# Kernel tuning notes

Measured on AMD Instinct MI355X. Metric: run time of the kernel, lower is better.

Reference implementation:

```python
import jax, jax.numpy as jnp
import numpy as np

NEG_SLOPE = 0.2
EPS = 1e-16


def _gat_conv(x, src, dst, edge_attr, W, We, att_src, att_dst, att_edge, bias):
    """PyG GATConv, heads=H, concat=False, edge_dim given. x:[N,F_in]."""
    N = x.shape[0]
    H, C = att_src.shape
    xs = (x @ W.T).reshape(N, H, C)                      # [N,H,C]
    a_src = jnp.einsum('nhc,hc->nh', xs, att_src)        # [N,H]
    a_dst = jnp.einsum('nhc,hc->nh', xs, att_dst)        # [N,H]
    e = (edge_attr @ We.T).reshape(-1, H, C)             # [E,H,C]
    a_edge = jnp.einsum('ehc,hc->eh', e, att_edge)       # [E,H]
    alpha = a_src[src] + a_dst[dst] + a_edge             # [E,H]
    alpha = jax.nn.leaky_relu(alpha, NEG_SLOPE)
    # segment softmax over destination nodes (per head)
    amax = jax.ops.segment_max(alpha, dst, num_segments=N)   # [N,H]
    ex = jnp.exp(alpha - amax[dst])
    denom = jax.ops.segment_sum(ex, dst, num_segments=N)     # [N,H]
    alpha = ex / (denom[dst] + EPS)
    msg = xs[src] * alpha[..., None]                     # [E,H,C]
    out = jax.ops.segment_sum(msg, dst, num_segments=N)  # [N,H,C]
    return out.mean(axis=1) + bias                       # concat=False -> mean over heads


def _add_self_loops(src, dst, edge_attr, N):
    # PyG add_self_loops with fill_value='mean': per-dst mean of incoming edge_attr
    ones = jnp.ones((edge_attr.shape[0],), edge_attr.dtype)
    sums = jax.ops.segment_sum(edge_attr, dst, num_segments=N)
    cnt = jax.ops.segment_sum(ones, dst, num_segments=N)
    loop_attr = sums / jnp.maximum(cnt, 1.0)[:, None]
    idx = jnp.arange(N, dtype=src.dtype)
    return (jnp.concatenate([src, idx]), jnp.concatenate([dst, idx]),
            jnp.concatenate([edge_attr, loop_attr], axis=0))


def setup_inputs() -> dict:
    key = jax.random.key(0)
    ks = jax.random.split(key, 16)
    N, E, F_IN, C, H = 100000, 1600000, 64, 32, 4
    s = 0.1
    inp = {
        'x': jax.random.normal(ks[0], (N, F_IN), jnp.float32),
        'edge_index': jax.random.randint(ks[1], (2, E), 0, N, jnp.int32),
        'edge_weight': jax.random.uniform(ks[2], (E, 1), jnp.float32),
        'w1': jax.random.normal(ks[3], (H * C, F_IN), jnp.float32) * s,
        'we1': jax.random.normal(ks[4], (H * C, 1), jnp.float32) * s,
        'as1': jax.random.normal(ks[5], (H, C), jnp.float32) * s,
        'ad1': jax.random.normal(ks[6], (H, C), jnp.float32) * s,
        'ae1': jax.random.normal(ks[7], (H, C), jnp.float32) * s,
        'b1': jnp.zeros((C,), jnp.float32),
        'w2': jax.random.normal(ks[8], (H * C, C), jnp.float32) * s,
        'we2': jax.random.normal(ks[9], (H * C, 1), jnp.float32) * s,
        'as2': jax.random.normal(ks[10], (H, C), jnp.float32) * s,
        'ad2': jax.random.normal(ks[11], (H, C), jnp.float32) * s,
        'ae2': jax.random.normal(ks[12], (H, C), jnp.float32) * s,
        'b2': jnp.zeros((C,), jnp.float32),
    }
    return inp


def reference(x, edge_index, edge_weight, w1, we1, as1, ad1, ae1, b1,
              w2, we2, as2, ad2, ae2, b2):
    N = x.shape[0]
    src, dst, ea = _add_self_loops(edge_index[0], edge_index[1], edge_weight, N)
    h = jax.nn.relu(_gat_conv(x, src, dst, ea, w1, we1, as1, ad1, ae1, b1))
    # nn.Dropout is identity in eval mode
    h = jax.nn.relu(_gat_conv(h, src, dst, ea, w2, we2, as2, ad2, ae2, b2))
    return h
```

## Files before the change

kernel.cpp:

```cpp
#include <hip/hip_runtime.h>
#include <hip/hip_fp16.h>
#include <cstddef>

#define GAT_EPS 1e-16f
#define CAP 48

__global__ __launch_bounds__(256, 2)
void k_gemm1h(const float* __restrict__ x, const float* __restrict__ W,
              const float* __restrict__ as_, const float* __restrict__ ad_,
              __half* __restrict__ xs, float* __restrict__ asrc,
              float* __restrict__ adst, int N, int gemmb,
              const int* __restrict__ src, const int* __restrict__ dst,
              const float* __restrict__ ew, int* __restrict__ cnt,
              int2* __restrict__ epk, int E,
              const float* __restrict__ we1, const float* __restrict__ ae1,
              const float* __restrict__ we2, const float* __restrict__ ae2,
              float* __restrict__ wd) {
    if (blockIdx.x == gridDim.x - 1) {
        int t = threadIdx.x;
        if (t < 128) {
            float v1 = we1[t] * ae1[t];
            float v2 = we2[t] * ae2[t];
#pragma unroll
            for (int off = 16; off; off >>= 1) {
                v1 += __shfl_xor(v1, off);
                v2 += __shfl_xor(v2, off);
            }
            if ((t & 31) == 0) { wd[t >> 5] = v1; wd[4 + (t >> 5)] = v2; }
        }
        return;
    }
    int g = blockIdx.x / 5;
    int r = blockIdx.x % 5;
    if (r != 0) {
        int i = (g * 4 + r - 1) * 256 + threadIdx.x;
        if (i < E) {
            int d = dst[i];
            int p = atomicAdd(&cnt[d], 1);
            p = min(p, CAP - 1);
            int2 q; q.x = src[i]; q.y = __float_as_int(ew[i]);
            epk[(size_t)d * CAP + p] = q;
        }
        return;
    }
    if (g >= gemmb) return;

    int n0 = g * 64;
    int t = threadIdx.x;
    int tx = t & 31;
    int ty = t >> 5;
    __shared__ __half Wh[64 * 132];
    __shared__ float xsh[64 * 65];
    int nrows = min(64, N - n0);
    for (int j = t; j < 8192; j += 256) {
        int c = j >> 6, k = j & 63;
        Wh[k * 132 + ((c & 31) << 2) + (c >> 5)] = __float2half(W[j]);
    }
    const float* xg = x + (size_t)n0 * 64;
    for (int j = t; j < nrows * 64; j += 256) xsh[(j >> 6) * 65 + (j & 63)] = xg[j];
    __syncthreads();

    float acc[8][4];
#pragma unroll
    for (int i = 0; i < 8; i++)
#pragma unroll
        for (int j = 0; j < 4; j++) acc[i][j] = 0.f;

#pragma unroll 4
    for (int k = 0; k < 64; k++) {
        const __half2* wp = reinterpret_cast<const __half2*>(&Wh[k * 132 + (tx << 2)]);
        float2 wf0 = __half22float2(wp[0]);
        float2 wf1 = __half22float2(wp[1]);
#pragma unroll
        for (int i = 0; i < 8; i++) {
            float xv = xsh[(ty * 8 + i) * 65 + k];
            acc[i][0] += xv * wf0.x;
            acc[i][1] += xv * wf0.y;
            acc[i][2] += xv * wf1.x;
            acc[i][3] += xv * wf1.y;
        }
    }

    float asv[4], adv[4];
#pragma unroll
    for (int j = 0; j < 4; j++) { asv[j] = as_[32 * j + tx]; adv[j] = ad_[32 * j + tx]; }

#pragma unroll
    for (int i = 0; i < 8; i++) {
        int row = ty * 8 + i;
        bool ok = row < nrows;
        __half* orow = xs + (size_t)(n0 + row) * 128;
#pragma unroll
        for (int j = 0; j < 4; j++) {
            if (ok) orow[32 * j + tx] = __float2half(acc[i][j]);
            float vs = acc[i][j] * asv[j];
            float vd = acc[i][j] * adv[j];
#pragma unroll
            for (int off = 16; off; off >>= 1) {
                vs += __shfl_xor(vs, off);
                vd += __shfl_xor(vd, off);
            }
            if (ok && tx == 0) {
                asrc[(size_t)(n0 + row) * 4 + j] = vs;
                adst[(size_t)(n0 + row) * 4 + j] = vd;
            }
        }
    }
}

__global__ __launch_bounds__(256, 2)
void k_gemm2(const float* __restrict__ h1, const float* __restrict__ W2,
             const float* __restrict__ as_, const float* __restrict__ ad_,
             __half* __restrict__ xs, float* __restrict__ asrc,
             float* __restrict__ adst, int N) {
    int n0 = blockIdx.x * 64;
    int t = threadIdx.x;
    int tx = t & 31;
    int ty = t >> 5;
    __shared__ __half Wh[32 * 132];
    __shared__ float xsh[64 * 33];
    int nrows = min(64, N - n0);
    for (int j = t; j < 4096; j += 256) {
        int c = j >> 5, k = j & 31;
        Wh[k * 132 + ((c & 31) << 2) + (c >> 5)] = __float2half(W2[j]);
    }
    const float* xg = h1 + (size_t)n0 * 32;
    for (int j = t; j < nrows * 32; j += 256) xsh[(j >> 5) * 33 + (j & 31)] = xg[j];
    __syncthreads();

    float acc[8][4];
#pragma unroll
    for (int i = 0; i < 8; i++)
#pragma unroll
        for (int j = 0; j < 4; j++) acc[i][j] = 0.f;

#pragma unroll 4
    for (int k = 0; k < 32; k++) {
        const __half2* wp = reinterpret_cast<const __half2*>(&Wh[k * 132 + (tx << 2)]);
        float2 wf0 = __half22float2(wp[0]);
        float2 wf1 = __half22float2(wp[1]);
#pragma unroll
        for (int i = 0; i < 8; i++) {
            float xv = xsh[(ty * 8 + i) * 33 + k];
            acc[i][0] += xv * wf0.x;
            acc[i][1] += xv * wf0.y;
            acc[i][2] += xv * wf1.x;
            acc[i][3] += xv * wf1.y;
        }
    }

    float asv[4], adv[4];
#pragma unroll
    for (int j = 0; j < 4; j++) { asv[j] = as_[32 * j + tx]; adv[j] = ad_[32 * j + tx]; }

#pragma unroll
    for (int i = 0; i < 8; i++) {
        int row = ty * 8 + i;
        bool ok = row < nrows;
        __half* orow = xs + (size_t)(n0 + row) * 128;
#pragma unroll
        for (int j = 0; j < 4; j++) {
            if (ok) orow[32 * j + tx] = __float2half(acc[i][j]);
            float vs = acc[i][j] * asv[j];
            float vd = acc[i][j] * adv[j];
#pragma unroll
            for (int off = 16; off; off >>= 1) {
                vs += __shfl_xor(vs, off);
                vd += __shfl_xor(vd, off);
            }
            if (ok && tx == 0) {
                asrc[(size_t)(n0 + row) * 4 + j] = vs;
                adst[(size_t)(n0 + row) * 4 + j] = vd;
            }
        }
    }
}

__global__ void k_gather(const int2* __restrict__ epk, const int* __restrict__ cnt,
                         const __half* __restrict__ xs,
                         const float* __restrict__ asrc, const float* __restrict__ adst,
                         const float* __restrict__ wedot, const float* __restrict__ bias,
                         float* __restrict__ out, int N) {
    int node = blockIdx.x * 4 + (threadIdx.x >> 6);
    if (node >= N) return;
    int l = threadIdx.x & 63;
    int q = l >> 4;
    int p = l & 15;
    int h = p >> 2;
    float wd = wedot[h];
    float ad = adst[(size_t)node * 4 + h];
    int cv = min(cnt[node], CAP);
    int beg = node * CAP;
    int end = beg + cv;

    float a0 = 0.f, a1 = 0.f, a2 = 0.f, a3 = 0.f;
    float a4 = 0.f, a5 = 0.f, a6 = 0.f, a7 = 0.f, ds = 0.f, easum = 0.f;
#pragma unroll 2
    for (int i = beg; i < end; i += 4) {
        int idx = i + q;
        bool valid = idx < end;
        int2 e = epk[valid ? idx : end - 1];
        int s = e.x;
        float eav = valid ? __int_as_float(e.y) : 0.f;
        easum += eav;
        float as = asrc[(size_t)s * 4 + h];
        float al = as + ad + __int_as_float(e.y) * wd;
        al = fmaxf(al, 0.2f * al);
        float w = valid ? __expf(al) : 0.f;
        uint4 raw = reinterpret_cast<const uint4*>(xs + (size_t)s * 128)[p];
        const __half2* hp = reinterpret_cast<const __half2*>(&raw);
        float2 f0 = __half22float2(hp[0]);
        float2 f1 = __half22float2(hp[1]);
        float2 f2 = __half22float2(hp[2]);
        float2 f3 = __half22float2(hp[3]);
        a0 += w * f0.x; a1 += w * f0.y;
        a2 += w * f1.x; a3 += w * f1.y;
        a4 += w * f2.x; a5 += w * f2.y;
        a6 += w * f3.x; a7 += w * f3.y;
        ds += w;
    }
    easum += __shfl_xor(easum, 16);
    easum += __shfl_xor(easum, 32);
    float loop_ea = easum / fmaxf((float)cv, 1.0f);
    float aln = asrc[(size_t)node * 4 + h] + ad + loop_ea * wd;
    aln = fmaxf(aln, 0.2f * aln);
    float wl = __expf(aln);
    if (q == 0) {
        uint4 raw = reinterpret_cast<const uint4*>(xs + (size_t)node * 128)[p];
        const __half2* hp = reinterpret_cast<const __half2*>(&raw);
        float2 f0 = __half22float2(hp[0]);
        float2 f1 = __half22float2(hp[1]);
        float2 f2 = __half22float2(hp[2]);
        float2 f3 = __half22float2(hp[3]);
        a0 += wl * f0.x; a1 += wl * f0.y;
        a2 += wl * f1.x; a3 += wl * f1.y;
        a4 += wl * f2.x; a5 += wl * f2.y;
        a6 += wl * f3.x; a7 += wl * f3.y;
        ds += wl;
    }
    a0 += __shfl_xor(a0, 16); a1 += __shfl_xor(a1, 16);
    a2 += __shfl_xor(a2, 16); a3 += __shfl_xor(a3, 16);
    a4 += __shfl_xor(a4, 16); a5 += __shfl_xor(a5, 16);
    a6 += __shfl_xor(a6, 16); a7 += __shfl_xor(a7, 16);
    ds += __shfl_xor(ds, 16);
    a0 += __shfl_xor(a0, 32); a1 += __shfl_xor(a1, 32);
    a2 += __shfl_xor(a2, 32); a3 += __shfl_xor(a3, 32);
    a4 += __shfl_xor(a4, 32); a5 += __shfl_xor(a5, 32);
    a6 += __shfl_xor(a6, 32); a7 += __shfl_xor(a7, 32);
    ds += __shfl_xor(ds, 32);
    float inv = 1.f / (ds + GAT_EPS);
    a0 *= inv; a1 *= inv; a2 *= inv; a3 *= inv;
    a4 *= inv; a5 *= inv; a6 *= inv; a7 *= inv;
    a0 += __shfl_xor(a0, 4); a1 += __shfl_xor(a1, 4);
    a2 += __shfl_xor(a2, 4); a3 += __shfl_xor(a3, 4);
    a4 += __shfl_xor(a4, 4); a5 += __shfl_xor(a5, 4);
    a6 += __shfl_xor(a6, 4); a7 += __shfl_xor(a7, 4);
    a0 += __shfl_xor(a0, 8); a1 += __shfl_xor(a1, 8);
    a2 += __shfl_xor(a2, 8); a3 += __shfl_xor(a3, 8);
    a4 += __shfl_xor(a4, 8); a5 += __shfl_xor(a5, 8);
    a6 += __shfl_xor(a6, 8); a7 += __shfl_xor(a7, 8);
    if (l < 4) {
        int c0 = l * 8;
        float4 r0, r1;
        r0.x = fmaxf(0.25f * a0 + bias[c0 + 0], 0.f);
        r0.y = fmaxf(0.25f * a1 + bias[c0 + 1], 0.f);
        r0.z = fmaxf(0.25f * a2 + bias[c0 + 2], 0.f);
        r0.w = fmaxf(0.25f * a3 + bias[c0 + 3], 0.f);
        r1.x = fmaxf(0.25f * a4 + bias[c0 + 4], 0.f);
        r1.y = fmaxf(0.25f * a5 + bias[c0 + 5], 0.f);
        r1.z = fmaxf(0.25f * a6 + bias[c0 + 6], 0.f);
        r1.w = fmaxf(0.25f * a7 + bias[c0 + 7], 0.f);
        float4* op = reinterpret_cast<float4*>(out + (size_t)node * 32 + c0);
        op[0] = r0;
        op[1] = r1;
    }
}

extern "C" void kernel_launch(void* const* d_in, const int* in_sizes, int n_in,
                              void* d_out, int out_size, void* d_ws, size_t ws_size,
                              hipStream_t stream) {
    const float* x   = (const float*)d_in[0];
    const int*   ei  = (const int*)d_in[1];
    const float* ewt = (const float*)d_in[2];
    const float* w1  = (const float*)d_in[3];
    const float* we1 = (const float*)d_in[4];
    const float* as1 = (const float*)d_in[5];
    const float* ad1 = (const float*)d_in[6];
    const float* ae1 = (const float*)d_in[7];
    const float* b1  = (const float*)d_in[8];
    const float* w2  = (const float*)d_in[9];
    const float* we2 = (const float*)d_in[10];
    const float* as2 = (const float*)d_in[11];
    const float* ad2 = (const float*)d_in[12];
    const float* ae2 = (const float*)d_in[13];
    const float* b2  = (const float*)d_in[14];

    const int N = in_sizes[0] / 64;
    const int E = in_sizes[1] / 2;
    const int* srcI = ei;
    const int* dstI = ei + E;

    char* base = (char*)d_ws;
    size_t off = 0;
    auto alloc = [&](size_t bytes) { char* p = base + off; off += (bytes + 15) & ~(size_t)15; return p; };
    __half* xs    = (__half*)alloc((size_t)N * 128 * sizeof(__half));
    float* h1     = (float*)alloc((size_t)N * 32 * sizeof(float));
    float* asrc   = (float*)alloc((size_t)N * 4 * sizeof(float));
    float* adst   = (float*)alloc((size_t)N * 4 * sizeof(float));
    int*   cnt    = (int*)alloc((size_t)N * sizeof(int));
    int2*  epk    = (int2*)alloc((size_t)N * CAP * sizeof(int2));
    float* wedot  = (float*)alloc(8 * sizeof(float));

    float* outF = (float*)d_out;

    hipMemsetAsync(cnt, 0, (size_t)N * sizeof(int), stream);

    const int gemmb = (N + 63) / 64;
    const int histb = (E + 255) / 256;
    const int G = gemmb > (histb + 3) / 4 ? gemmb : (histb + 3) / 4;
    const int gb = (N + 3) / 4;

    k_gemm1h<<<5 * G + 1, 256, 0, stream>>>(x, w1, as1, ad1, xs, asrc, adst, N, gemmb,
                                            srcI, dstI, ewt, cnt, epk, E,
                                            we1, ae1, we2, ae2, wedot);

    k_gather<<<gb, 256, 0, stream>>>(epk, cnt, xs, asrc, adst,
                                     wedot + 0, b1, h1, N);

    k_gemm2<<<gemmb, 256, 0, stream>>>(h1, w2, as2, ad2, xs, asrc, adst, N);
    k_gather<<<gb, 256, 0, stream>>>(epk, cnt, xs, asrc, adst,
                                     wedot + 4, b2, outF, N);
}
```

Baseline: 319.1 us.

## Eliminate layer-2 GEMM by aggregating 32-dim h1 then projecting per node

Removes the k_gemm2 kernel. Layer-2 attention logits are computed from h1 using precombined vectors W2^T·att, folded into the layer-1 gather epilogue. Layer 2 then gathers only the 32-dim fp16 h1 per edge, weighted per head, and applies W2 once per node after aggregation, since aggregation and projection are both linear. This drops one kernel launch and cuts per-edge gather traffic from 128 halves to 32, at the cost of a per-block shared-memory W2 load and a shuffle-heavy projection in the gather.

```diff
diff --git a/kernel.cpp b/kernel.cpp
--- a/kernel.cpp
+++ b/kernel.cpp
@@ -15,7 +15,10 @@
               int2* __restrict__ epk, int E,
               const float* __restrict__ we1, const float* __restrict__ ae1,
               const float* __restrict__ we2, const float* __restrict__ ae2,
-              float* __restrict__ wd) {
+              float* __restrict__ wd,
+              const float* __restrict__ as2, const float* __restrict__ ad2,
+              const float* __restrict__ W2, float* __restrict__ vs2,
+              float* __restrict__ vd2) {
     if (blockIdx.x == gridDim.x - 1) {
         int t = threadIdx.x;
         if (t < 128) {
@@ -27,6 +30,15 @@
                 v2 += __shfl_xor(v2, off);
             }
             if ((t & 31) == 0) { wd[t >> 5] = v1; wd[4 + (t >> 5)] = v2; }
+            int h = t >> 5, c = t & 31;
+            float s = 0.f, dv = 0.f;
+            for (int k = 0; k < 32; k++) {
+                float w = W2[(h * 32 + k) * 32 + c];
+                s  += as2[h * 32 + k] * w;
+                dv += ad2[h * 32 + k] * w;
+            }
+            vs2[t] = s;
+            vd2[t] = dv;
         }
         return;
     }
@@ -108,79 +120,13 @@
     }
 }
 
-__global__ __launch_bounds__(256, 2)
-void k_gemm2(const float* __restrict__ h1, const float* __restrict__ W2,
-             const float* __restrict__ as_, const float* __restrict__ ad_,
-             __half* __restrict__ xs, float* __restrict__ asrc,
-             float* __restrict__ adst, int N) {
-    int n0 = blockIdx.x * 64;
-    int t = threadIdx.x;
-    int tx = t & 31;
-    int ty = t >> 5;
-    __shared__ __half Wh[32 * 132];
-    __shared__ float xsh[64 * 33];
-    int nrows = min(64, N - n0);
-    for (int j = t; j < 4096; j += 256) {
-        int c = j >> 5, k = j & 31;
-        Wh[k * 132 + ((c & 31) << 2) + (c >> 5)] = __float2half(W2[j]);
-    }
-    const float* xg = h1 + (size_t)n0 * 32;
-    for (int j = t; j < nrows * 32; j += 256) xsh[(j >> 5) * 33 + (j & 31)] = xg[j];
-    __syncthreads();
-
-    float acc[8][4];
-#pragma unroll
-    for (int i = 0; i < 8; i++)
-#pragma unroll
-        for (int j = 0; j < 4; j++) acc[i][j] = 0.f;
-
-#pragma unroll 4
-    for (int k = 0; k < 32; k++) {
-        const __half2* wp = reinterpret_cast<const __half2*>(&Wh[k * 132 + (tx << 2)]);
-        float2 wf0 = __half22float2(wp[0]);
-        float2 wf1 = __half22float2(wp[1]);
-#pragma unroll
-        for (int i = 0; i < 8; i++) {
-            float xv = xsh[(ty * 8 + i) * 33 + k];
-            acc[i][0] += xv * wf0.x;
-            acc[i][1] += xv * wf0.y;
-            acc[i][2] += xv * wf1.x;
-            acc[i][3] += xv * wf1.y;
-        }
-    }
-
-    float asv[4], adv[4];
-#pragma unroll
-    for (int j = 0; j < 4; j++) { asv[j] = as_[32 * j + tx]; adv[j] = ad_[32 * j + tx]; }
-
-#pragma unroll
-    for (int i = 0; i < 8; i++) {
-        int row = ty * 8 + i;
-        bool ok = row < nrows;
-        __half* orow = xs + (size_t)(n0 + row) * 128;
-#pragma unroll
-        for (int j = 0; j < 4; j++) {
-            if (ok) orow[32 * j + tx] = __float2half(acc[i][j]);
-            float vs = acc[i][j] * asv[j];
-            float vd = acc[i][j] * adv[j];
-#pragma unroll
-            for (int off = 16; off; off >>= 1) {
-                vs += __shfl_xor(vs, off);
-                vd += __shfl_xor(vd, off);
-            }
-            if (ok && tx == 0) {
-                asrc[(size_t)(n0 + row) * 4 + j] = vs;
-                adst[(size_t)(n0 + row) * 4 + j] = vd;
-            }
-        }
-    }
-}
-
-__global__ void k_gather(const int2* __restrict__ epk, const int* __restrict__ cnt,
-                         const __half* __restrict__ xs,
-                         const float* __restrict__ asrc, const float* __restrict__ adst,
-                         const float* __restrict__ wedot, const float* __restrict__ bias,
-                         float* __restrict__ out, int N) {
+__global__ void k_gather1(const int2* __restrict__ epk, const int* __restrict__ cnt,
+                          const __half* __restrict__ xs,
+                          const float* __restrict__ asrc, const float* __restrict__ adst,
+                          const float* __restrict__ wedot, const float* __restrict__ bias,
+                          const float* __restrict__ vs2, const float* __restrict__ vd2,
+                          __half2* __restrict__ h1, float* __restrict__ asrc2,
+                          float* __restrict__ adst2, int N) {
     int node = blockIdx.x * 4 + (threadIdx.x >> 6);
     if (node >= N) return;
     int l = threadIdx.x & 63;
@@ -261,18 +207,157 @@
     a6 += __shfl_xor(a6, 8); a7 += __shfl_xor(a7, 8);
     if (l < 4) {
         int c0 = l * 8;
-        float4 r0, r1;
-        r0.x = fmaxf(0.25f * a0 + bias[c0 + 0], 0.f);
-        r0.y = fmaxf(0.25f * a1 + bias[c0 + 1], 0.f);
-        r0.z = fmaxf(0.25f * a2 + bias[c0 + 2], 0.f);
-        r0.w = fmaxf(0.25f * a3 + bias[c0 + 3], 0.f);
-        r1.x = fmaxf(0.25f * a4 + bias[c0 + 4], 0.f);
-        r1.y = fmaxf(0.25f * a5 + bias[c0 + 5], 0.f);
-        r1.z = fmaxf(0.25f * a6 + bias[c0 + 6], 0.f);
-        r1.w = fmaxf(0.25f * a7 + bias[c0 + 7], 0.f);
-        float4* op = reinterpret_cast<float4*>(out + (size_t)node * 32 + c0);
-        op[0] = r0;
-        op[1] = r1;
+        float rv[8];
+        rv[0] = fmaxf(0.25f * a0 + bias[c0 + 0], 0.f);
+        rv[1] = fmaxf(0.25f * a1 + bias[c0 + 1], 0.f);
+        rv[2] = fmaxf(0.25f * a2 + bias[c0 + 2], 0.f);
+        rv[3] = fmaxf(0.25f * a3 + bias[c0 + 3], 0.f);
+        rv[4] = fmaxf(0.25f * a4 + bias[c0 + 4], 0.f);
+        rv[5] = fmaxf(0.25f * a5 + bias[c0 + 5], 0.f);
+        rv[6] = fmaxf(0.25f * a6 + bias[c0 + 6], 0.f);
+        rv[7] = fmaxf(0.25f * a7 + bias[c0 + 7], 0.f);
+        __half2* hp = h1 + (size_t)node * 16 + l * 4;
+        hp[0] = __floats2half2_rn(rv[0], rv[1]);
+        hp[1] = __floats2half2_rn(rv[2], rv[3]);
+        hp[2] = __floats2half2_rn(rv[4], rv[5]);
+        hp[3] = __floats2half2_rn(rv[6], rv[7]);
+        float pa[4] = {0.f, 0.f, 0.f, 0.f}, pd[4] = {0.f, 0.f, 0.f, 0.f};
+#pragma unroll
+        for (int hh = 0; hh < 4; hh++)
+#pragma unroll
+            for (int j = 0; j < 8; j++) {
+                pa[hh] += rv[j] * vs2[hh * 32 + c0 + j];
+                pd[hh] += rv[j] * vd2[hh * 32 + c0 + j];
+            }
+#pragma unroll
+        for (int hh = 0; hh < 4; hh++) {
+            pa[hh] += __shfl_xor(pa[hh], 1);
+            pa[hh] += __shfl_xor(pa[hh], 2);
+            pd[hh] += __shfl_xor(pd[hh], 1);
+            pd[hh] += __shfl_xor(pd[hh], 2);
+        }
+        if (l == 0) {
+            float4 wa, wb;
+            wa.x = pa[0]; wa.y = pa[1]; wa.z = pa[2]; wa.w = pa[3];
+            wb.x = pd[0]; wb.y = pd[1]; wb.z = pd[2]; wb.w = pd[3];
+            *reinterpret_cast<float4*>(asrc2 + (size_t)node * 4) = wa;
+            *reinterpret_cast<float4*>(adst2 + (size_t)node * 4) = wb;
+        }
+    }
+}
+
+__global__ void k_gather2(const int2* __restrict__ epk, const int* __restrict__ cnt,
+                          const __half2* __restrict__ h1,
+                          const float* __restrict__ asrc, const float* __restrict__ adst,
+                          const float* __restrict__ wedot, const float* __restrict__ W2,
+                          const float* __restrict__ bias, float* __restrict__ out, int N) {
+    __shared__ unsigned int Wsh[2180];
+    int t = threadIdx.x;
+    for (int j = t; j < 2048; j += 256) {
+        int rr = j >> 4, kk = j & 15;
+        __half2 hv = __floats2half2_rn(W2[rr * 32 + 2 * kk], W2[rr * 32 + 2 * kk + 1]);
+        Wsh[rr * 17 + (rr >> 5) + kk] = *reinterpret_cast<unsigned int*>(&hv);
+    }
+    __syncthreads();
+    int node = blockIdx.x * 4 + (t >> 6);
+    if (node >= N) return;
+    int l = t & 63;
+    int q = l >> 4;
+    int p = l & 15;
+    int h = l & 3;
+    int base = l & 48;
+    float wd = wedot[h];
+    float ad = adst[(size_t)node * 4 + h];
+    int cv = min(cnt[node], CAP);
+    int beg = node * CAP;
+    int end = beg + cv;
+
+    float g00 = 0.f, g01 = 0.f, g10 = 0.f, g11 = 0.f;
+    float g20 = 0.f, g21 = 0.f, g30 = 0.f, g31 = 0.f;
+    float ds = 0.f, easum = 0.f;
+#pragma unroll 2
+    for (int i = beg; i < end; i += 4) {
+        int idx = i + q;
+        bool valid = idx < end;
+        int2 e = epk[valid ? idx : end - 1];
+        int s = e.x;
+        float eav = valid ? __int_as_float(e.y) : 0.f;
+        easum += eav;
+        float as = asrc[(size_t)s * 4 + h];
+        float al = as + ad + __int_as_float(e.y) * wd;
+        al = fmaxf(al, 0.2f * al);
+        float w = valid ? __expf(al) : 0.f;
+        float w0 = __shfl(w, base | 0);
+        float w1 = __shfl(w, base | 1);
+        float w2v = __shfl(w, base | 2);
+        float w3 = __shfl(w, base | 3);
+        float2 f = __half22float2(h1[(size_t)s * 16 + p]);
+        g00 += w0 * f.x; g01 += w0 * f.y;
+        g10 += w1 * f.x; g11 += w1 * f.y;
+        g20 += w2v * f.x; g21 += w2v * f.y;
+        g30 += w3 * f.x; g31 += w3 * f.y;
+        ds += w;
+    }
+    easum += __shfl_xor(easum, 16);
+    easum += __shfl_xor(easum, 32);
+    float loop_ea = easum / fmaxf((float)cv, 1.0f);
+    float aln = asrc[(size_t)node * 4 + h] + ad + loop_ea * wd;
+    aln = fmaxf(aln, 0.2f * aln);
+    float wl = __expf(aln);
+    float wl0 = __shfl(wl, base | 0);
+    float wl1 = __shfl(wl, base | 1);
+    float wl2 = __shfl(wl, base | 2);
+    float wl3 = __shfl(wl, base | 3);
+    if (q == 0) {
+        float2 f = __half22float2(h1[(size_t)node * 16 + p]);
+        g00 += wl0 * f.x; g01 += wl0 * f.y;
+        g10 += wl1 * f.x; g11 += wl1 * f.y;
+        g20 += wl2 * f.x; g21 += wl2 * f.y;
+        g30 += wl3 * f.x; g31 += wl3 * f.y;
+        ds += wl;
+    }
+    g00 += __shfl_xor(g00, 16); g01 += __shfl_xor(g01, 16);
+    g10 += __shfl_xor(g10, 16); g11 += __shfl_xor(g11, 16);
+    g20 += __shfl_xor(g20, 16); g21 += __shfl_xor(g21, 16);
+    g30 += __shfl_xor(g30, 16); g31 += __shfl_xor(g31, 16);
+    g00 += __shfl_xor(g00, 32); g01 += __shfl_xor(g01, 32);
+    g10 += __shfl_xor(g10, 32); g11 += __shfl_xor(g11, 32);
+    g20 += __shfl_xor(g20, 32); g21 += __shfl_xor(g21, 32);
+    g30 += __shfl_xor(g30, 32); g31 += __shfl_xor(g31, 32);
+    ds += __shfl_xor(ds, 4);
+    ds += __shfl_xor(ds, 8);
+    ds += __shfl_xor(ds, 16);
+    ds += __shfl_xor(ds, 32);
+    float inv_own = 1.f / (0.25f * ds + GAT_EPS);
+    float invq = __shfl(inv_own, base | q);
+    float gq0, gq1;
+    if (q == 0)      { gq0 = g00; gq1 = g01; }
+    else if (q == 1) { gq0 = g10; gq1 = g11; }
+    else if (q == 2) { gq0 = g20; gq1 = g21; }
+    else             { gq0 = g30; gq1 = g31; }
+    int rowA17 = ((q << 5) + (p << 1)) * 17 + q;
+    float oA = 0.f, oB = 0.f;
+#pragma unroll
+    for (int kk = 0; kk < 16; kk++) {
+        float glo = __shfl(gq0, base | kk);
+        float ghi = __shfl(gq1, base | kk);
+        unsigned ua = Wsh[rowA17 + kk];
+        unsigned ub = Wsh[rowA17 + 17 + kk];
+        float2 wa = __half22float2(*reinterpret_cast<__half2*>(&ua));
+        float2 wb = __half22float2(*reinterpret_cast<__half2*>(&ub));
+        oA += glo * wa.x + ghi * wa.y;
+        oB += glo * wb.x + ghi * wb.y;
+    }
+    oA *= invq; oB *= invq;
+    oA += __shfl_xor(oA, 16);
+    oA += __shfl_xor(oA, 32);
+    oB += __shfl_xor(oB, 16);
+    oB += __shfl_xor(oB, 32);
+    if (q == 0) {
+        float2 r;
+        r.x = fmaxf(0.25f * oA + bias[2 * p], 0.f);
+        r.y = fmaxf(0.25f * oB + bias[2 * p + 1], 0.f);
+        *reinterpret_cast<float2*>(out + (size_t)node * 32 + 2 * p) = r;
     }
 }
 
@@ -303,13 +388,17 @@
     char* base = (char*)d_ws;
     size_t off = 0;
     auto alloc = [&](size_t bytes) { char* p = base + off; off += (bytes + 15) & ~(size_t)15; return p; };
-    __half* xs    = (__half*)alloc((size_t)N * 128 * sizeof(__half));
-    float* h1     = (float*)alloc((size_t)N * 32 * sizeof(float));
-    float* asrc   = (float*)alloc((size_t)N * 4 * sizeof(float));
-    float* adst   = (float*)alloc((size_t)N * 4 * sizeof(float));
-    int*   cnt    = (int*)alloc((size_t)N * sizeof(int));
-    int2*  epk    = (int2*)alloc((size_t)N * CAP * sizeof(int2));
-    float* wedot  = (float*)alloc(8 * sizeof(float));
+    __half* xs     = (__half*)alloc((size_t)N * 128 * sizeof(__half));
+    __half2* h1    = (__half2*)alloc((size_t)N * 16 * sizeof(__half2));
+    float* asrc    = (float*)alloc((size_t)N * 4 * sizeof(float));
+    float* adst    = (float*)alloc((size_t)N * 4 * sizeof(float));
+    float* asrc2   = (float*)alloc((size_t)N * 4 * sizeof(float));
+    float* adst2   = (float*)alloc((size_t)N * 4 * sizeof(float));
+    int*   cnt     = (int*)alloc((size_t)N * sizeof(int));
+    int2*  epk     = (int2*)alloc((size_t)N * CAP * sizeof(int2));
+    float* wedot   = (float*)alloc(8 * sizeof(float));
+    float* vs2     = (float*)alloc(128 * sizeof(float));
+    float* vd2     = (float*)alloc(128 * sizeof(float));
 
     float* outF = (float*)d_out;
 
@@ -322,12 +411,12 @@
 
     k_gemm1h<<<5 * G + 1, 256, 0, stream>>>(x, w1, as1, ad1, xs, asrc, adst, N, gemmb,
                                             srcI, dstI, ewt, cnt, epk, E,
-                                            we1, ae1, we2, ae2, wedot);
-
-    k_gather<<<gb, 256, 0, stream>>>(epk, cnt, xs, asrc, adst,
-                                     wedot + 0, b1, h1, N);
-
-    k_gemm2<<<gemmb, 256, 0, stream>>>(h1, w2, as2, ad2, xs, asrc, adst, N);
-    k_gather<<<gb, 256, 0, stream>>>(epk, cnt, xs, asrc, adst,
-                                     wedot + 4, b2, outF, N);
+                                            we1, ae1, we2, ae2, wedot,
+                                            as2, ad2, w2, vs2, vd2);
+
+    k_gather1<<<gb, 256, 0, stream>>>(epk, cnt, xs, asrc, adst,
+                                      wedot + 0, b1, vs2, vd2, h1, asrc2, adst2, N);
+
+    k_gather2<<<gb, 256, 0, stream>>>(epk, cnt, h1, asrc2, adst2,
+                                      wedot + 4, w2, b2, outF, N);
 }
```

New measurement: 343.3 us. 1.08x slower.
